# Kernel tuning notes

Hardware: AMD Instinct MI355X
Metric: run time of the kernel (lower is better)

The kernel has to match this reference:

```python
import jax, jax.numpy as jnp
import numpy as np

INPUT_SIZE = 32
HIDDEN = 128
OUT_SIZE = 1
B, S = 256, 1200


def _gru_layer(x_seq, W_ih, W_hh, b_ih, b_hh):
    """PyTorch-convention GRU layer. x_seq: [B,S,D] -> [B,S,H].
    W_ih: [3H,D], W_hh: [3H,H], gate order (r,z,n)."""
    Bsz = x_seq.shape[0]
    H = W_hh.shape[1]
    # Precompute input projections for all timesteps (one big GEMM).
    gates_x = jnp.einsum('bsd,gd->bsg', x_seq, W_ih) + b_ih  # [B,S,3H]

    def step(h, gx):
        gh = h @ W_hh.T + b_hh                 # [B,3H]
        xr, xz, xn = jnp.split(gx, 3, axis=-1)
        hr, hz, hn = jnp.split(gh, 3, axis=-1)
        r = jax.nn.sigmoid(xr + hr)
        z = jax.nn.sigmoid(xz + hz)
        n = jnp.tanh(xn + r * hn)
        h_new = (1.0 - z) * n + z * h
        return h_new, h_new

    h0 = jnp.zeros((Bsz, H), x_seq.dtype)
    _, ys = jax.lax.scan(step, h0, jnp.swapaxes(gates_x, 0, 1))  # [S,B,H]
    return jnp.swapaxes(ys, 0, 1)


def setup_inputs() -> dict:
    key = jax.random.key(0)
    ks = jax.random.split(key, 12)
    s_in = 1.0 / np.sqrt(HIDDEN)  # PyTorch GRU init scale
    d = {
        'x': jax.random.normal(ks[0], (B, S, INPUT_SIZE), dtype=jnp.float32),
        'W_ih0': jax.random.uniform(ks[1], (3 * HIDDEN, INPUT_SIZE), jnp.float32, -s_in, s_in),
        'W_hh0': jax.random.uniform(ks[2], (3 * HIDDEN, HIDDEN), jnp.float32, -s_in, s_in),
        'b_ih0': jax.random.uniform(ks[3], (3 * HIDDEN,), jnp.float32, -s_in, s_in),
        'b_hh0': jax.random.uniform(ks[4], (3 * HIDDEN,), jnp.float32, -s_in, s_in),
        'W_ih1': jax.random.uniform(ks[5], (3 * HIDDEN, HIDDEN), jnp.float32, -s_in, s_in),
        'W_hh1': jax.random.uniform(ks[6], (3 * HIDDEN, HIDDEN), jnp.float32, -s_in, s_in),
        'b_ih1': jax.random.uniform(ks[7], (3 * HIDDEN,), jnp.float32, -s_in, s_in),
        'b_hh1': jax.random.uniform(ks[8], (3 * HIDDEN,), jnp.float32, -s_in, s_in),
        'W_lin': jax.random.uniform(ks[9], (OUT_SIZE, HIDDEN), jnp.float32, -s_in, s_in),
        'b_lin': jax.random.uniform(ks[10], (OUT_SIZE,), jnp.float32, -s_in, s_in),
    }
    return d


def reference(x, W_ih0, W_hh0, b_ih0, b_hh0, W_ih1, W_hh1, b_ih1, b_hh1, W_lin, b_lin):
    h1 = _gru_layer(x, W_ih0, W_hh0, b_ih0, b_hh0)   # [B,S,H]  (dropout inactive at eval)
    h2 = _gru_layer(h1, W_ih1, W_hh1, b_ih1, b_hh1)  # [B,S,H]
    out = jax.nn.relu(h2)
    out = jnp.einsum('bsh,oh->bso', out, W_lin) + b_lin  # [B,S,OUT_SIZE]
    return out.reshape(-1, 12)
```

## Files before the change

### kernel.cpp

```cpp
#include <hip/hip_runtime.h>
#include <hip/hip_bf16.h>


typedef _Float16 h2 __attribute__((ext_vector_type(2)));

#if __has_builtin(__builtin_amdgcn_fdot2)
__device__ __forceinline__ float dot2f(h2 a, h2 b, float c) {
  return __builtin_amdgcn_fdot2(a, b, c, false);
}
#else
__device__ __forceinline__ float dot2f(h2 a, h2 b, float c) {
  return c + (float)a[0] * (float)b[0] + (float)a[1] * (float)b[1];
}
#endif

__device__ __forceinline__ h2 pack2(float x, float y) {
  h2 r; r[0] = (_Float16)x; r[1] = (_Float16)y; return r;
}
__device__ __forceinline__ float sigm(float x) {
  return 1.0f / (1.0f + __expf(-x));
}
__device__ __forceinline__ float tanh_f(float x) {
  x = fminf(fmaxf(x, -15.f), 15.f);
  float e = __expf(2.f * x);
  return (e - 1.f) / (e + 1.f);
}
__device__ __forceinline__ float hsum(float4 v) { return (v.x + v.y) + (v.z + v.w); }

__device__ __forceinline__ void load_pack8(const float* p, h2* w) {
  float4 a = ((const float4*)p)[0], b = ((const float4*)p)[1];
  w[0] = pack2(a.x, a.y); w[1] = pack2(a.z, a.w);
  w[2] = pack2(b.x, b.y); w[3] = pack2(b.z, b.w);
}

#define SEQ 1200
#define HID 128
#define INSZ 32

#define DOT4Q(W, F, ACC)                                                \
  ACC = dot2f((W)[0], __builtin_bit_cast(h2, (F).x), ACC);              \
  ACC = dot2f((W)[1], __builtin_bit_cast(h2, (F).y), ACC);              \
  ACC = dot2f((W)[2], __builtin_bit_cast(h2, (F).z), ACC);              \
  ACC = dot2f((W)[3], __builtin_bit_cast(h2, (F).w), ACC);

#define DOT8(W, FA, FB, ACC)                                            \
  DOT4Q(&(W)[0], FA, ACC) DOT4Q(&(W)[4], FB, ACC)

__global__ __launch_bounds__(1024) void gru_fused(
    const float* __restrict__ x,
    const float* __restrict__ Wih0, const float* __restrict__ Whh0,
    const float* __restrict__ bih0, const float* __restrict__ bhh0,
    const float* __restrict__ Wih1, const float* __restrict__ Whh1,
    const float* __restrict__ bih1, const float* __restrict__ bhh1,
    const float* __restrict__ Wlin, const float* __restrict__ blin,
    float* __restrict__ out)
{
  const int tid = threadIdx.x;
  const int b   = blockIdx.x;
  const int oct = tid >> 3;
  const int ko  = tid & 7;

  __shared__ float G1p[4 * 1024];
  __shared__ float G2p[4 * 1024];
  __shared__ float  s0f[HID], s1f[HID];
  __shared__ float4 s0h4[16], s1h4[16];
  __shared__ float4 xh[2][4];
  __shared__ float  pbf[32];

  h2 wi0[3][2];
  h2 wh0[3][8];
  h2 wi1[3][8];
  h2 wh1[3][8];
#pragma unroll
  for (int rr = 0; rr < 3; ++rr) {
    const int row = rr * HID + oct;
    float4 v = *(const float4*)(Wih0 + (size_t)row * INSZ + ko * 4);
    wi0[rr][0] = pack2(v.x, v.y); wi0[rr][1] = pack2(v.z, v.w);
#pragma unroll
    for (int c = 0; c < 2; ++c) {
      load_pack8(Whh0 + (size_t)row * HID + ko * 16 + c * 8, &wh0[rr][c * 4]);
      load_pack8(Wih1 + (size_t)row * HID + ko * 16 + c * 8, &wi1[rr][c * 4]);
      load_pack8(Whh1 + (size_t)row * HID + ko * 16 + c * 8, &wh1[rr][c * 4]);
    }
  }

  float bA = 0.f, bB = 0.f, bC = 0.f, bD = 0.f, wl = 0.f;
  if (tid < 128) {
    bA = bih1[tid] + bhh1[tid];
    bB = bih1[HID + tid] + bhh1[HID + tid];
    bC = bih1[2 * HID + tid];
    bD = bhh1[2 * HID + tid];
    wl = Wlin[tid];
  } else if (tid < 256) {
    const int i = tid - 128;
    bA = bih0[i] + bhh0[i];
    bB = bih0[HID + i] + bhh0[HID + i];
    bC = bih0[2 * HID + i];
    bD = bhh0[2 * HID + i];
  }
  const float blv = blin[0];

  if (tid < HID) { s0f[tid] = 0.f; s1f[tid] = 0.f; }
  if (tid < 64) { ((float*)s0h4)[tid] = 0.f; ((float*)s1h4)[tid] = 0.f; }
  const float2* xsrc = (const float2*)x + (size_t)b * SEQ * (INSZ / 2);
  if (tid < 16) {
    float2 v = xsrc[tid];
    ((h2*)xh[0])[tid] = pack2(v.x, v.y);
  }
  __syncthreads();

  float* outp = out + (size_t)b * SEQ;

  for (int t = -1; t < SEQ; ++t) {
    {
      const int buf = (t + 1) & 1;
      const float2 xq = ((const float2*)xh[buf])[ko];
      const h2 x0 = __builtin_bit_cast(h2, xq.x);
      const h2 x1 = __builtin_bit_cast(h2, xq.y);
      const float4 sA = s0h4[ko * 2], sB = s0h4[ko * 2 + 1];
      const float4 tA = s1h4[ko * 2], tB = s1h4[ko * 2 + 1];
      float a0 = 0.f, a1 = 0.f, a2 = 0.f, a3 = 0.f;
      a0 = dot2f(wi0[0][0], x0, a0); a0 = dot2f(wi0[0][1], x1, a0);
      DOT8(wh0[0], sA, sB, a0)
      a1 = dot2f(wi0[1][0], x0, a1); a1 = dot2f(wi0[1][1], x1, a1);
      DOT8(wh0[1], sA, sB, a1)
      a2 = dot2f(wi0[2][0], x0, a2); a2 = dot2f(wi0[2][1], x1, a2);
      DOT8(wh0[2], sA, sB, a3)
      float c0 = 0.f, c1 = 0.f, c2 = 0.f, c3 = 0.f;
      DOT8(wi1[0], sA, sB, c0) DOT8(wh1[0], tA, tB, c0)
      DOT8(wi1[1], sA, sB, c1) DOT8(wh1[1], tA, tB, c1)
      DOT8(wi1[2], sA, sB, c2)
      DOT8(wh1[2], tA, tB, c3)
      G1p[tid] = a0; G1p[1024 + tid] = a1; G1p[2048 + tid] = a2; G1p[3072 + tid] = a3;
      G2p[tid] = c0; G2p[1024 + tid] = c1; G2p[2048 + tid] = c2; G2p[3072 + tid] = c3;
    }
    float2 xn;
    if ((tid & ~15) == 256) {
      const int ti = (t + 2 < SEQ) ? t + 2 : SEQ - 1;
      xn = xsrc[(size_t)ti * 16 + (tid - 256)];
    }
    __syncthreads();

    if (tid < 128) {
      if (t >= 0) {
        const float4* G4 = (const float4*)G2p;
        float ra = hsum(G4[2 * tid])       + hsum(G4[2 * tid + 1]);
        float za = hsum(G4[256 + 2 * tid]) + hsum(G4[257 + 2 * tid]);
        float xa = hsum(G4[512 + 2 * tid]) + hsum(G4[513 + 2 * tid]);
        float ha = hsum(G4[768 + 2 * tid]) + hsum(G4[769 + 2 * tid]);
        float r = sigm(ra + bA);
        float z = sigm(za + bB);
        float n = tanh_f(xa + bC + r * (ha + bD));
        float h = (1.f - z) * n + z * s1f[tid];
        s1f[tid] = h;
        ((_Float16*)s1h4)[tid] = (_Float16)h;
        float p = fmaxf(h, 0.f) * wl;
        p += __shfl_xor(p, 1, 64);
        p += __shfl_xor(p, 2, 64);
        p += __shfl_xor(p, 4, 64);
        if ((tid & 7) == 0) pbf[(t & 1) * 16 + (tid >> 3)] = p;
      }
    } else if (tid < 256) {
      const int i = tid - 128;
      const float4* G4 = (const float4*)G1p;
      float ra = hsum(G4[2 * i])       + hsum(G4[2 * i + 1]);
      float za = hsum(G4[256 + 2 * i]) + hsum(G4[257 + 2 * i]);
      float xa = hsum(G4[512 + 2 * i]) + hsum(G4[513 + 2 * i]);
      float ha = hsum(G4[768 + 2 * i]) + hsum(G4[769 + 2 * i]);
      float r = sigm(ra + bA);
      float z = sigm(za + bB);
      float n = tanh_f(xa + bC + r * (ha + bD));
      float h = (1.f - z) * n + z * s0f[i];
      s0f[i] = h;
      ((_Float16*)s0h4)[i] = (_Float16)h;
    } else if (tid < 272) {
      ((h2*)xh[t & 1])[tid - 256] = pack2(xn.x, xn.y);
    } else if (tid == 320 && t >= 1) {
      const float4* p4 = (const float4*)(pbf + ((t - 1) & 1) * 16);
      outp[t - 1] = hsum(p4[0]) + hsum(p4[1]) + hsum(p4[2]) + hsum(p4[3]) + blv;
    }
    __syncthreads();
  }

  if (tid == 0) {
    const float4* p4 = (const float4*)(pbf + ((SEQ - 1) & 1) * 16);
    outp[SEQ - 1] = hsum(p4[0]) + hsum(p4[1]) + hsum(p4[2]) + hsum(p4[3]) + blv;
  }
}

extern "C" void kernel_launch(void* const* d_in, const int* in_sizes, int n_in,
                              void* d_out, int out_size, void* d_ws, size_t ws_size,
                              hipStream_t stream) {
  const float* x    = (const float*)d_in[0];
  const float* Wih0 = (const float*)d_in[1];
  const float* Whh0 = (const float*)d_in[2];
  const float* bih0 = (const float*)d_in[3];
  const float* bhh0 = (const float*)d_in[4];
  const float* Wih1 = (const float*)d_in[5];
  const float* Whh1 = (const float*)d_in[6];
  const float* bih1 = (const float*)d_in[7];
  const float* bhh1 = (const float*)d_in[8];
  const float* Wlin = (const float*)d_in[9];
  const float* blin = (const float*)d_in[10];
  float* outp = (float*)d_out;

  const int Bn = in_sizes[0] / (SEQ * INSZ);
  hipLaunchKernelGGL(gru_fused, dim3(Bn), dim3(1024), 0, stream,
                     x, Wih0, Whh0, bih0, bhh0,
                     Wih1, Whh1, bih1, bhh1, Wlin, blin, outp);
}
```

Baseline: 1.447 ms.

## Pad partial-sum LDS layout, force one block per CU, use inline dot2 asm

The per-thread partial sums are now stored with a stride of 9 per output row, so the reducing threads read with padding instead of float4 vectors. This is meant to cut LDS bank conflicts. A large dummy LDS array plus launch_bounds(1024,1) forces one block per CU, apparently to give the scheduler or caches more room. The fdot2 builtin is replaced by inline v_dot2_f32_f16 asm. The cost is scalar LDS reads in the reduction, lower occupancy, and asm that hides the operation from compiler scheduling.

```diff
diff --git a/kernel.cpp b/kernel.cpp
--- a/kernel.cpp
+++ b/kernel.cpp
@@ -4,15 +4,10 @@
 
 typedef _Float16 h2 __attribute__((ext_vector_type(2)));
 
-#if __has_builtin(__builtin_amdgcn_fdot2)
 __device__ __forceinline__ float dot2f(h2 a, h2 b, float c) {
-  return __builtin_amdgcn_fdot2(a, b, c, false);
-}
-#else
-__device__ __forceinline__ float dot2f(h2 a, h2 b, float c) {
-  return c + (float)a[0] * (float)b[0] + (float)a[1] * (float)b[1];
-}
-#endif
+  asm("v_dot2_f32_f16 %0, %1, %2, %0" : "+v"(c) : "v"(a), "v"(b));
+  return c;
+}
 
 __device__ __forceinline__ h2 pack2(float x, float y) {
   h2 r; r[0] = (_Float16)x; r[1] = (_Float16)y; return r;
@@ -25,7 +20,6 @@
   float e = __expf(2.f * x);
   return (e - 1.f) / (e + 1.f);
 }
-__device__ __forceinline__ float hsum(float4 v) { return (v.x + v.y) + (v.z + v.w); }
 
 __device__ __forceinline__ void load_pack8(const float* p, h2* w) {
   float4 a = ((const float4*)p)[0], b = ((const float4*)p)[1];
@@ -36,6 +30,7 @@
 #define SEQ 1200
 #define HID 128
 #define INSZ 32
+#define GS 1152
 
 #define DOT4Q(W, F, ACC)                                                \
   ACC = dot2f((W)[0], __builtin_bit_cast(h2, (F).x), ACC);              \
@@ -46,7 +41,7 @@
 #define DOT8(W, FA, FB, ACC)                                            \
   DOT4Q(&(W)[0], FA, ACC) DOT4Q(&(W)[4], FB, ACC)
 
-__global__ __launch_bounds__(1024) void gru_fused(
+__global__ __launch_bounds__(1024, 1) void gru_fused(
     const float* __restrict__ x,
     const float* __restrict__ Wih0, const float* __restrict__ Whh0,
     const float* __restrict__ bih0, const float* __restrict__ bhh0,
@@ -60,12 +55,13 @@
   const int oct = tid >> 3;
   const int ko  = tid & 7;
 
-  __shared__ float G1p[4 * 1024];
-  __shared__ float G2p[4 * 1024];
+  __shared__ float G1p[4 * GS];
+  __shared__ float G2p[4 * GS];
   __shared__ float  s0f[HID], s1f[HID];
   __shared__ float4 s0h4[16], s1h4[16];
   __shared__ float4 xh[2][4];
   __shared__ float  pbf[32];
+  __shared__ float ldspad[11264];
 
   h2 wi0[3][2];
   h2 wh0[3][8];
@@ -99,6 +95,11 @@
     bD = bhh0[2 * HID + i];
   }
   const float blv = blin[0];
+
+  if (tid == 1023) {
+    volatile float* vp = ldspad;
+    vp[0] = blv;
+  }
 
   if (tid < HID) { s0f[tid] = 0.f; s1f[tid] = 0.f; }
   if (tid < 64) { ((float*)s0h4)[tid] = 0.f; ((float*)s1h4)[tid] = 0.f; }
@@ -131,8 +132,9 @@
       DOT8(wi1[1], sA, sB, c1) DOT8(wh1[1], tA, tB, c1)
       DOT8(wi1[2], sA, sB, c2)
       DOT8(wh1[2], tA, tB, c3)
-      G1p[tid] = a0; G1p[1024 + tid] = a1; G1p[2048 + tid] = a2; G1p[3072 + tid] = a3;
-      G2p[tid] = c0; G2p[1024 + tid] = c1; G2p[2048 + tid] = c2; G2p[3072 + tid] = c3;
+      const int gb = oct * 9 + ko;
+      G1p[gb] = a0; G1p[GS + gb] = a1; G1p[2 * GS + gb] = a2; G1p[3 * GS + gb] = a3;
+      G2p[gb] = c0; G2p[GS + gb] = c1; G2p[2 * GS + gb] = c2; G2p[3 * GS + gb] = c3;
     }
     float2 xn;
     if ((tid & ~15) == 256) {
@@ -143,11 +145,15 @@
 
     if (tid < 128) {
       if (t >= 0) {
-        const float4* G4 = (const float4*)G2p;
-        float ra = hsum(G4[2 * tid])       + hsum(G4[2 * tid + 1]);
-        float za = hsum(G4[256 + 2 * tid]) + hsum(G4[257 + 2 * tid]);
-        float xa = hsum(G4[512 + 2 * tid]) + hsum(G4[513 + 2 * tid]);
-        float ha = hsum(G4[768 + 2 * tid]) + hsum(G4[769 + 2 * tid]);
+        const int gb = tid * 9;
+        float ra = 0.f, za = 0.f, xa = 0.f, ha = 0.f;
+#pragma unroll
+        for (int j = 0; j < 8; ++j) {
+          ra += G2p[gb + j];
+          za += G2p[GS + gb + j];
+          xa += G2p[2 * GS + gb + j];
+          ha += G2p[3 * GS + gb + j];
+        }
         float r = sigm(ra + bA);
         float z = sigm(za + bB);
         float n = tanh_f(xa + bC + r * (ha + bD));
@@ -162,11 +168,15 @@
       }
     } else if (tid < 256) {
       const int i = tid - 128;
-      const float4* G4 = (const float4*)G1p;
-      float ra = hsum(G4[2 * i])       + hsum(G4[2 * i + 1]);
-      float za = hsum(G4[256 + 2 * i]) + hsum(G4[257 + 2 * i]);
-      float xa = hsum(G4[512 + 2 * i]) + hsum(G4[513 + 2 * i]);
-      float ha = hsum(G4[768 + 2 * i]) + hsum(G4[769 + 2 * i]);
+      const int gb = i * 9;
+      float ra = 0.f, za = 0.f, xa = 0.f, ha = 0.f;
+#pragma unroll
+      for (int j = 0; j < 8; ++j) {
+        ra += G1p[gb + j];
+        za += G1p[GS + gb + j];
+        xa += G1p[2 * GS + gb + j];
+        ha += G1p[3 * GS + gb + j];
+      }
       float r = sigm(ra + bA);
       float z = sigm(za + bB);
       float n = tanh_f(xa + bC + r * (ha + bD));
@@ -177,14 +187,18 @@
       ((h2*)xh[t & 1])[tid - 256] = pack2(xn.x, xn.y);
     } else if (tid == 320 && t >= 1) {
       const float4* p4 = (const float4*)(pbf + ((t - 1) & 1) * 16);
-      outp[t - 1] = hsum(p4[0]) + hsum(p4[1]) + hsum(p4[2]) + hsum(p4[3]) + blv;
+      float4 u = p4[0], v = p4[1], w = p4[2], s = p4[3];
+      outp[t - 1] = (u.x + u.y + u.z + u.w) + (v.x + v.y + v.z + v.w) +
+                    (w.x + w.y + w.z + w.w) + (s.x + s.y + s.z + s.w) + blv;
     }
     __syncthreads();
   }
 
   if (tid == 0) {
     const float4* p4 = (const float4*)(pbf + ((SEQ - 1) & 1) * 16);
-    outp[SEQ - 1] = hsum(p4[0]) + hsum(p4[1]) + hsum(p4[2]) + hsum(p4[3]) + blv;
+    float4 u = p4[0], v = p4[1], w = p4[2], s = p4[3];
+    outp[SEQ - 1] = (u.x + u.y + u.z + u.w) + (v.x + v.y + v.z + v.w) +
+                    (w.x + w.y + w.z + w.w) + (s.x + s.y + s.z + s.w) + blv;
   }
 }
 
```

After: 1.569 ms. +8.4%, slower.

## Split fused two-layer GRU into per-layer kernels with shuffle reductions

Applied to the files above, without the earlier changes.

Replaces the single wavefront-pipelined kernel that ran both GRU layers together with two kernels: layer 1 writes its fp16 hidden sequence to workspace, and layer 2 reads it back and applies ReLU plus the linear head. Each kernel reduces partial dot products with intra-wave shuffles instead of staging partials in shared memory, which removes one __syncthreads per step and the big LDS partial buffers. The cost is a global-memory round trip for the layer-1 outputs and two serialized 1200-step recurrences instead of one overlapped loop, so the sequential step count per batch roughly doubles.

```diff
diff --git a/kernel.cpp b/kernel.cpp
--- a/kernel.cpp
+++ b/kernel.cpp
@@ -25,8 +25,6 @@
   float e = __expf(2.f * x);
   return (e - 1.f) / (e + 1.f);
 }
-__device__ __forceinline__ float hsum(float4 v) { return (v.x + v.y) + (v.z + v.w); }
-
 __device__ __forceinline__ void load_pack8(const float* p, h2* w) {
   float4 a = ((const float4*)p)[0], b = ((const float4*)p)[1];
   w[0] = pack2(a.x, a.y); w[1] = pack2(a.z, a.w);
@@ -46,10 +44,85 @@
 #define DOT8(W, FA, FB, ACC)                                            \
   DOT4Q(&(W)[0], FA, ACC) DOT4Q(&(W)[4], FB, ACC)
 
-__global__ __launch_bounds__(1024) void gru_fused(
+#define RED8(A) \
+  A += __shfl_xor(A, 1, 64); A += __shfl_xor(A, 2, 64); A += __shfl_xor(A, 4, 64);
+
+__global__ __launch_bounds__(1024) void gru_l1(
     const float* __restrict__ x,
     const float* __restrict__ Wih0, const float* __restrict__ Whh0,
     const float* __restrict__ bih0, const float* __restrict__ bhh0,
+    unsigned short* __restrict__ h1g)
+{
+  const int tid = threadIdx.x;
+  const int b   = blockIdx.x;
+  const int o   = tid >> 3;
+  const int ko  = tid & 7;
+
+  __shared__ _Float16 s0h[2][HID];
+  __shared__ _Float16 xh[2][INSZ];
+
+  h2 wi0[3][2];
+  h2 wh0[3][8];
+#pragma unroll
+  for (int rr = 0; rr < 3; ++rr) {
+    const int row = rr * HID + o;
+    float4 v = *(const float4*)(Wih0 + (size_t)row * INSZ + ko * 4);
+    wi0[rr][0] = pack2(v.x, v.y); wi0[rr][1] = pack2(v.z, v.w);
+    load_pack8(Whh0 + (size_t)row * HID + ko * 16,     &wh0[rr][0]);
+    load_pack8(Whh0 + (size_t)row * HID + ko * 16 + 8, &wh0[rr][4]);
+  }
+  const float bA = bih0[o] + bhh0[o];
+  const float bB = bih0[HID + o] + bhh0[HID + o];
+  const float bC = bih0[2 * HID + o];
+  const float bD = bhh0[2 * HID + o];
+
+  float hprev = 0.f;
+  if (tid < 64) ((float*)s0h[0])[tid] = 0.f;
+  const float2* xsrc = (const float2*)x + (size_t)b * SEQ * (INSZ / 2);
+  if (tid < 16) { float2 v = xsrc[tid]; ((h2*)xh[0])[tid] = pack2(v.x, v.y); }
+  __syncthreads();
+
+  unsigned short* hout = h1g + (size_t)b * SEQ * HID;
+
+  for (int t = 0; t < SEQ; ++t) {
+    const int rb = t & 1, wb = rb ^ 1;
+    float2 xn;
+    const bool ldx = (ko == 1) && (o < 16);
+    if (ldx) xn = xsrc[(size_t)((t + 1 < SEQ) ? t + 1 : SEQ - 1) * 16 + o];
+
+    const float2 xv = ((const float2*)xh[rb])[ko];
+    const h2 x0 = __builtin_bit_cast(h2, xv.x);
+    const h2 x1 = __builtin_bit_cast(h2, xv.y);
+    const float4 sA = ((const float4*)s0h[rb])[ko * 2];
+    const float4 sB = ((const float4*)s0h[rb])[ko * 2 + 1];
+
+    float a0 = 0.f, a1 = 0.f, a2 = 0.f, a3 = 0.f;
+    a0 = dot2f(wi0[0][0], x0, a0); a0 = dot2f(wi0[0][1], x1, a0);
+    DOT8(wh0[0], sA, sB, a0)
+    a1 = dot2f(wi0[1][0], x0, a1); a1 = dot2f(wi0[1][1], x1, a1);
+    DOT8(wh0[1], sA, sB, a1)
+    a2 = dot2f(wi0[2][0], x0, a2); a2 = dot2f(wi0[2][1], x1, a2);
+    DOT8(wh0[2], sA, sB, a3)
+    RED8(a0) RED8(a1) RED8(a2) RED8(a3)
+
+    if (ko == 0) {
+      float r = sigm(a0 + bA);
+      float z = sigm(a1 + bB);
+      float n = tanh_f(a2 + bC + r * (a3 + bD));
+      float h = (1.f - z) * n + z * hprev;
+      hprev = h;
+      const _Float16 hf = (_Float16)h;
+      s0h[wb][o] = hf;
+      hout[(size_t)t * HID + o] = __builtin_bit_cast(unsigned short, hf);
+    } else if (ldx) {
+      ((h2*)xh[wb])[o] = pack2(xn.x, xn.y);
+    }
+    __syncthreads();
+  }
+}
+
+__global__ __launch_bounds__(1024) void gru_l2(
+    const unsigned short* __restrict__ h1g,
     const float* __restrict__ Wih1, const float* __restrict__ Whh1,
     const float* __restrict__ bih1, const float* __restrict__ bhh1,
     const float* __restrict__ Wlin, const float* __restrict__ blin,
@@ -57,134 +130,86 @@
 {
   const int tid = threadIdx.x;
   const int b   = blockIdx.x;
-  const int oct = tid >> 3;
+  const int o   = tid >> 3;
   const int ko  = tid & 7;
 
-  __shared__ float G1p[4 * 1024];
-  __shared__ float G2p[4 * 1024];
-  __shared__ float  s0f[HID], s1f[HID];
-  __shared__ float4 s0h4[16], s1h4[16];
-  __shared__ float4 xh[2][4];
-  __shared__ float  pbf[32];
-
-  h2 wi0[3][2];
-  h2 wh0[3][8];
+  __shared__ _Float16 s1h[2][HID];
+  __shared__ _Float16 hb[2][HID];
+  __shared__ float    pbf[2][16];
+
   h2 wi1[3][8];
   h2 wh1[3][8];
 #pragma unroll
   for (int rr = 0; rr < 3; ++rr) {
-    const int row = rr * HID + oct;
-    float4 v = *(const float4*)(Wih0 + (size_t)row * INSZ + ko * 4);
-    wi0[rr][0] = pack2(v.x, v.y); wi0[rr][1] = pack2(v.z, v.w);
-#pragma unroll
-    for (int c = 0; c < 2; ++c) {
-      load_pack8(Whh0 + (size_t)row * HID + ko * 16 + c * 8, &wh0[rr][c * 4]);
-      load_pack8(Wih1 + (size_t)row * HID + ko * 16 + c * 8, &wi1[rr][c * 4]);
-      load_pack8(Whh1 + (size_t)row * HID + ko * 16 + c * 8, &wh1[rr][c * 4]);
+    const int row = rr * HID + o;
+    load_pack8(Wih1 + (size_t)row * HID + ko * 16,     &wi1[rr][0]);
+    load_pack8(Wih1 + (size_t)row * HID + ko * 16 + 8, &wi1[rr][4]);
+    load_pack8(Whh1 + (size_t)row * HID + ko * 16,     &wh1[rr][0]);
+    load_pack8(Whh1 + (size_t)row * HID + ko * 16 + 8, &wh1[rr][4]);
+  }
+  const float bA = bih1[o] + bhh1[o];
+  const float bB = bih1[HID + o] + bhh1[HID + o];
+  const float bC = bih1[2 * HID + o];
+  const float bD = bhh1[2 * HID + o];
+  const float wl  = Wlin[o];
+  const float blv = blin[0];
+
+  float hprev = 0.f;
+  if (tid < 64) ((float*)s1h[0])[tid] = 0.f;
+  const uint4* hsrc = (const uint4*)(h1g + (size_t)b * SEQ * HID);
+  if (tid < 16) ((uint4*)hb[0])[tid] = hsrc[tid];
+  __syncthreads();
+
+  float* outp = out + (size_t)b * SEQ;
+
+  for (int t = 0; t < SEQ; ++t) {
+    const int rb = t & 1, wb = rb ^ 1;
+    uint4 hn;
+    const bool ldh = (ko == 1) && (o < 16);
+    if (ldh) hn = hsrc[(size_t)((t + 1 < SEQ) ? t + 1 : SEQ - 1) * 16 + o];
+
+    const float4 hA = ((const float4*)hb[rb])[ko * 2];
+    const float4 hB = ((const float4*)hb[rb])[ko * 2 + 1];
+    const float4 sA = ((const float4*)s1h[rb])[ko * 2];
+    const float4 sB = ((const float4*)s1h[rb])[ko * 2 + 1];
+
+    float a0 = 0.f, a1 = 0.f, a2 = 0.f, a3 = 0.f;
+    DOT8(wi1[0], hA, hB, a0) DOT8(wh1[0], sA, sB, a0)
+    DOT8(wi1[1], hA, hB, a1) DOT8(wh1[1], sA, sB, a1)
+    DOT8(wi1[2], hA, hB, a2)
+    DOT8(wh1[2], sA, sB, a3)
+    RED8(a0) RED8(a1) RED8(a2) RED8(a3)
+
+    float p = 0.f;
+    if (ko == 0) {
+      float r = sigm(a0 + bA);
+      float z = sigm(a1 + bB);
+      float n = tanh_f(a2 + bC + r * (a3 + bD));
+      float h = (1.f - z) * n + z * hprev;
+      hprev = h;
+      s1h[wb][o] = (_Float16)h;
+      p = fmaxf(h, 0.f) * wl;
+    } else if (ldh) {
+      ((uint4*)hb[wb])[o] = hn;
     }
-  }
-
-  float bA = 0.f, bB = 0.f, bC = 0.f, bD = 0.f, wl = 0.f;
-  if (tid < 128) {
-    bA = bih1[tid] + bhh1[tid];
-    bB = bih1[HID + tid] + bhh1[HID + tid];
-    bC = bih1[2 * HID + tid];
-    bD = bhh1[2 * HID + tid];
-    wl = Wlin[tid];
-  } else if (tid < 256) {
-    const int i = tid - 128;
-    bA = bih0[i] + bhh0[i];
-    bB = bih0[HID + i] + bhh0[HID + i];
-    bC = bih0[2 * HID + i];
-    bD = bhh0[2 * HID + i];
-  }
-  const float blv = blin[0];
-
-  if (tid < HID) { s0f[tid] = 0.f; s1f[tid] = 0.f; }
-  if (tid < 64) { ((float*)s0h4)[tid] = 0.f; ((float*)s1h4)[tid] = 0.f; }
-  const float2* xsrc = (const float2*)x + (size_t)b * SEQ * (INSZ / 2);
-  if (tid < 16) {
-    float2 v = xsrc[tid];
-    ((h2*)xh[0])[tid] = pack2(v.x, v.y);
-  }
-  __syncthreads();
-
-  float* outp = out + (size_t)b * SEQ;
-
-  for (int t = -1; t < SEQ; ++t) {
-    {
-      const int buf = (t + 1) & 1;
-      const float2 xq = ((const float2*)xh[buf])[ko];
-      const h2 x0 = __builtin_bit_cast(h2, xq.x);
-      const h2 x1 = __builtin_bit_cast(h2, xq.y);
-      const float4 sA = s0h4[ko * 2], sB = s0h4[ko * 2 + 1];
-      const float4 tA = s1h4[ko * 2], tB = s1h4[ko * 2 + 1];
-      float a0 = 0.f, a1 = 0.f, a2 = 0.f, a3 = 0.f;
-      a0 = dot2f(wi0[0][0], x0, a0); a0 = dot2f(wi0[0][1], x1, a0);
-      DOT8(wh0[0], sA, sB, a0)
-      a1 = dot2f(wi0[1][0], x0, a1); a1 = dot2f(wi0[1][1], x1, a1);
-      DOT8(wh0[1], sA, sB, a1)
-      a2 = dot2f(wi0[2][0], x0, a2); a2 = dot2f(wi0[2][1], x1, a2);
-      DOT8(wh0[2], sA, sB, a3)
-      float c0 = 0.f, c1 = 0.f, c2 = 0.f, c3 = 0.f;
-      DOT8(wi1[0], sA, sB, c0) DOT8(wh1[0], tA, tB, c0)
-      DOT8(wi1[1], sA, sB, c1) DOT8(wh1[1], tA, tB, c1)
-      DOT8(wi1[2], sA, sB, c2)
-      DOT8(wh1[2], tA, tB, c3)
-      G1p[tid] = a0; G1p[1024 + tid] = a1; G1p[2048 + tid] = a2; G1p[3072 + tid] = a3;
-      G2p[tid] = c0; G2p[1024 + tid] = c1; G2p[2048 + tid] = c2; G2p[3072 + tid] = c3;
-    }
-    float2 xn;
-    if ((tid & ~15) == 256) {
-      const int ti = (t + 2 < SEQ) ? t + 2 : SEQ - 1;
-      xn = xsrc[(size_t)ti * 16 + (tid - 256)];
+    p += __shfl_xor(p, 8, 64);
+    p += __shfl_xor(p, 16, 64);
+    p += __shfl_xor(p, 32, 64);
+    if ((tid & 63) == 0) pbf[rb][tid >> 6] = p;
+    if (tid == 2 && t >= 1) {
+      float s = 0.f;
+#pragma unroll
+      for (int j = 0; j < 16; ++j) s += pbf[wb][j];
+      outp[t - 1] = s + blv;
     }
     __syncthreads();
-
-    if (tid < 128) {
-      if (t >= 0) {
-        const float4* G4 = (const float4*)G2p;
-        float ra = hsum(G4[2 * tid])       + hsum(G4[2 * tid + 1]);
-        float za = hsum(G4[256 + 2 * tid]) + hsum(G4[257 + 2 * tid]);
-        float xa = hsum(G4[512 + 2 * tid]) + hsum(G4[513 + 2 * tid]);
-        float ha = hsum(G4[768 + 2 * tid]) + hsum(G4[769 + 2 * tid]);
-        float r = sigm(ra + bA);
-        float z = sigm(za + bB);
-        float n = tanh_f(xa + bC + r * (ha + bD));
-        float h = (1.f - z) * n + z * s1f[tid];
-        s1f[tid] = h;
-        ((_Float16*)s1h4)[tid] = (_Float16)h;
-        float p = fmaxf(h, 0.f) * wl;
-        p += __shfl_xor(p, 1, 64);
-        p += __shfl_xor(p, 2, 64);
-        p += __shfl_xor(p, 4, 64);
-        if ((tid & 7) == 0) pbf[(t & 1) * 16 + (tid >> 3)] = p;
-      }
-    } else if (tid < 256) {
-      const int i = tid - 128;
-      const float4* G4 = (const float4*)G1p;
-      float ra = hsum(G4[2 * i])       + hsum(G4[2 * i + 1]);
-      float za = hsum(G4[256 + 2 * i]) + hsum(G4[257 + 2 * i]);
-      float xa = hsum(G4[512 + 2 * i]) + hsum(G4[513 + 2 * i]);
-      float ha = hsum(G4[768 + 2 * i]) + hsum(G4[769 + 2 * i]);
-      float r = sigm(ra + bA);
-      float z = sigm(za + bB);
-      float n = tanh_f(xa + bC + r * (ha + bD));
-      float h = (1.f - z) * n + z * s0f[i];
-      s0f[i] = h;
-      ((_Float16*)s0h4)[i] = (_Float16)h;
-    } else if (tid < 272) {
-      ((h2*)xh[t & 1])[tid - 256] = pack2(xn.x, xn.y);
-    } else if (tid == 320 && t >= 1) {
-      const float4* p4 = (const float4*)(pbf + ((t - 1) & 1) * 16);
-      outp[t - 1] = hsum(p4[0]) + hsum(p4[1]) + hsum(p4[2]) + hsum(p4[3]) + blv;
-    }
-    __syncthreads();
-  }
-
-  if (tid == 0) {
-    const float4* p4 = (const float4*)(pbf + ((SEQ - 1) & 1) * 16);
-    outp[SEQ - 1] = hsum(p4[0]) + hsum(p4[1]) + hsum(p4[2]) + hsum(p4[3]) + blv;
+  }
+
+  if (tid == 2) {
+    float s = 0.f;
+#pragma unroll
+    for (int j = 0; j < 16; ++j) s += pbf[(SEQ - 1) & 1][j];
+    outp[SEQ - 1] = s + blv;
   }
 }
 
@@ -205,7 +230,10 @@
   float* outp = (float*)d_out;
 
   const int Bn = in_sizes[0] / (SEQ * INSZ);
-  hipLaunchKernelGGL(gru_fused, dim3(Bn), dim3(1024), 0, stream,
-                     x, Wih0, Whh0, bih0, bhh0,
-                     Wih1, Whh1, bih1, bhh1, Wlin, blin, outp);
-}
+  unsigned short* h1g = (unsigned short*)d_ws;
+
+  hipLaunchKernelGGL(gru_l1, dim3(Bn), dim3(1024), 0, stream,
+                     x, Wih0, Whh0, bih0, bhh0, h1g);
+  hipLaunchKernelGGL(gru_l2, dim3(Bn), dim3(1024), 0, stream,
+                     h1g, Wih1, Whh1, bih1, bhh1, Wlin, blin, outp);
+}
```

Result: slower. 2.577 ms (+78.1%).
